# Kernel optimization log

Hardware: AMD Instinct MI355X
Metric: run time of the kernel (lower is better)

The kernel has to match this reference:

```python
import jax, jax.numpy as jnp
import numpy as np

B, T, I, H, O = 64, 1024, 512, 768, 512


def setup_inputs() -> dict:
    key = jax.random.key(0)
    ks = jax.random.split(key, 8)
    x_seq = jax.random.normal(ks[0], (B, T, I), dtype=jnp.float32)
    s = 0.02
    # Gate order along the 4H axis: f, i, g, o (matches the torch module's gates).
    Wx_f = jax.random.normal(ks[1], (4 * H, I), dtype=jnp.float32) * s
    Wh_f = jax.random.normal(ks[2], (4 * H, H), dtype=jnp.float32) * s
    Wx_b = jax.random.normal(ks[3], (4 * H, I), dtype=jnp.float32) * s
    Wh_b = jax.random.normal(ks[4], (4 * H, H), dtype=jnp.float32) * s
    # forget-gate bias init to 1.0 (f_Wxf.bias / b_Wxf.bias), rest 0
    b_gate = jnp.concatenate([jnp.ones((H,), jnp.float32), jnp.zeros((3 * H,), jnp.float32)])
    b_f = b_gate
    b_b = b_gate
    Why = jax.random.normal(ks[5], (O, 2 * H), dtype=jnp.float32) * s
    by = jnp.zeros((O,), jnp.float32)
    return {"x_seq": x_seq, "Wx_f": Wx_f, "Wh_f": Wh_f, "b_f": b_f,
            "Wx_b": Wx_b, "Wh_b": Wh_b, "b_b": b_b, "Why": Why, "by": by}


def _lstm_dir(x, Wx, Wh, b):
    # Precompute all input-to-gate projections in one fused GEMM over time.
    xp = jnp.einsum('bti,gi->btg', x, Wx) + b  # (B, T, 4H)

    def step(carry, xp_t):
        h, c = carry
        z = xp_t + h @ Wh.T                     # (B, 4H)
        f = jax.nn.sigmoid(z[:, 0 * H:1 * H])
        i = jax.nn.sigmoid(z[:, 1 * H:2 * H])
        g = jnp.tanh(z[:, 2 * H:3 * H])
        o = jax.nn.sigmoid(z[:, 3 * H:4 * H])
        c = f * c + i * g
        h = o * jnp.tanh(c)
        return (h, c), None

    h0 = jnp.zeros((x.shape[0], H), x.dtype)
    c0 = jnp.zeros((x.shape[0], H), x.dtype)
    (h, c), _ = jax.lax.scan(step, (h0, c0), jnp.swapaxes(xp, 0, 1))
    return h, c


def reference(x_seq, Wx_f, Wh_f, b_f, Wx_b, Wh_b, b_b, Why, by):
    h_fwd, c_fwd = _lstm_dir(x_seq, Wx_f, Wh_f, b_f)
    h_bwd, c_bwd = _lstm_dir(x_seq[:, ::-1, :], Wx_b, Wh_b, b_b)
    h_combined = jnp.concatenate([h_fwd, h_bwd], axis=1)  # (B, 2H)
    out = h_combined @ Why.T + by
    return out, h_fwd, c_fwd, h_bwd, c_bwd
```

## Files before the change

kernel.cpp:

```cpp
#include <hip/hip_runtime.h>
#include <hip/hip_cooperative_groups.h>

namespace cg = cooperative_groups;

#define B_ 64
#define T_ 1024
#define I_ 512
#define H_ 768
#define O_ 512
#define G4 3072
#define JB 16
#define NJ 48
#define NWGS 192

typedef short short8 __attribute__((ext_vector_type(8)));
typedef float f32x4 __attribute__((ext_vector_type(4)));
typedef int int4v __attribute__((ext_vector_type(4)));

#define XBF_BYTES  (67108864)
#define WCAT_BYTES (15728640)
#define HBUF_BYTES (393216)

__device__ __forceinline__ unsigned short f32_to_bf16(float f) {
    union { float f; unsigned int u; } v; v.f = f;
    unsigned int r = v.u + 0x7fffu + ((v.u >> 16) & 1u);
    return (unsigned short)(r >> 16);
}
__device__ __forceinline__ float sigmoid_f(float x) { return 1.0f / (1.0f + __expf(-x)); }
__device__ __forceinline__ float tanh_f(float x) {
    float e = __expf(2.0f * x);
    return 1.0f - 2.0f / (e + 1.0f);
}

__device__ __forceinline__ void glds16(const void* g, void* l) {
    __builtin_amdgcn_global_load_lds(
        (const __attribute__((address_space(1))) unsigned int*)g,
        (__attribute__((address_space(3))) unsigned int*)l, 16, 0, 0);
}

__device__ __forceinline__ void ldsbar() {
    asm volatile("s_waitcnt lgkmcnt(0)" ::: "memory");
    __builtin_amdgcn_sched_barrier(0);
    __builtin_amdgcn_s_barrier();
    __builtin_amdgcn_sched_barrier(0);
}

__global__ void prep_x_kernel(const float* __restrict__ x, unsigned short* __restrict__ xb) {
    const size_t n = (size_t)B_ * T_ * 64;
    for (size_t i = (size_t)blockIdx.x * blockDim.x + threadIdx.x; i < n;
         i += (size_t)gridDim.x * blockDim.x) {
        int b  = (int)(i >> 16);
        int t  = (int)((i >> 6) & 1023);
        int kb = (int)(i & 63);
        const float4 v0 = *(const float4*)(x + i * 8);
        const float4 v1 = *(const float4*)(x + i * 8 + 4);
        short8 o;
        o[0] = (short)f32_to_bf16(v0.x); o[1] = (short)f32_to_bf16(v0.y);
        o[2] = (short)f32_to_bf16(v0.z); o[3] = (short)f32_to_bf16(v0.w);
        o[4] = (short)f32_to_bf16(v1.x); o[5] = (short)f32_to_bf16(v1.y);
        o[6] = (short)f32_to_bf16(v1.z); o[7] = (short)f32_to_bf16(v1.w);
        *(short8*)(xb + (((size_t)t * 64 + kb) * 64 + b) * 8) = o;
    }
}

__global__ void prep_w_kernel(const float* __restrict__ Wx_f, const float* __restrict__ Wh_f,
                              const float* __restrict__ Wx_b, const float* __restrict__ Wh_b,
                              unsigned short* __restrict__ w2, unsigned short* __restrict__ h2,
                              unsigned* __restrict__ bar) {
    const size_t n = (size_t)2 * G4 * 160;
    for (size_t i = (size_t)blockIdx.x * blockDim.x + threadIdx.x; i < n;
         i += (size_t)gridDim.x * blockDim.x) {
        int dir = (int)(i / 491520);
        int r2  = (int)(i % 491520);
        int row = r2 / 160;
        int kb  = r2 % 160;
        const float* Wx = dir ? Wx_b : Wx_f;
        const float* Wh = dir ? Wh_b : Wh_f;
        const float* src = (kb < 64) ? (Wx + (size_t)row * I_ + kb * 8)
                                     : (Wh + (size_t)row * H_ + (kb - 64) * 8);
        const float4 v0 = *(const float4*)(src);
        const float4 v1 = *(const float4*)(src + 4);
        short8 o;
        o[0] = (short)f32_to_bf16(v0.x); o[1] = (short)f32_to_bf16(v0.y);
        o[2] = (short)f32_to_bf16(v0.z); o[3] = (short)f32_to_bf16(v0.w);
        o[4] = (short)f32_to_bf16(v1.x); o[5] = (short)f32_to_bf16(v1.y);
        o[6] = (short)f32_to_bf16(v1.z); o[7] = (short)f32_to_bf16(v1.w);
        *(short8*)(w2 + (((size_t)dir * 160 + kb) * G4 + row) * 8) = o;
        if (i < 24576) {
            short8 z = {0,0,0,0,0,0,0,0};
            *(short8*)(h2 + i * 8) = z;
        }
        if (i < 512) bar[i] = 0u;
    }
}

__global__ void __launch_bounds__(512, 1)
bilstm_kernel(const float* __restrict__ bias_f, const float* __restrict__ bias_b,
              const unsigned short* __restrict__ xb, const unsigned short* __restrict__ w2,
              unsigned short* h2, unsigned* bar, float* d_out) {
    __shared__ unsigned short x_lds[64 * 32 * 8];
    __shared__ unsigned short h_lds[96 * 32 * 8];
    __shared__ float z_lds[4][32][17];
    __shared__ float c_tile[32][16];

    const int tid   = threadIdx.x;
    const int wg    = blockIdx.x;
    const int dir   = wg / 96;
    const int rem   = wg % 96;
    const int bh    = rem / NJ;
    const int jb    = rem % NJ;
    const int j0    = jb * JB;
    const int wave  = tid >> 6;
    const int lane  = tid & 63;
    const int gate  = wave & 3;
    const int mhalf = wave >> 2;
    const int quad  = lane >> 4;
    const int lrow  = lane & 15;
    const int m0l   = mhalf * 16 + lrow;

    c_tile[tid >> 4][tid & 15] = 0.0f;

    const float bias_r = (dir ? bias_b : bias_f)[gate * H_ + j0 + lrow];
    const int wrow = gate * H_ + j0 + lrow;

    short8 wxr[16];
#pragma unroll
    for (int ks = 0; ks < 16; ++ks)
        wxr[ks] = *(const short8*)(w2 + (((size_t)dir * 160 + ks * 4 + quad) * G4 + wrow) * 8);
    short8 wh[24];
#pragma unroll
    for (int ks = 0; ks < 24; ++ks)
        wh[ks] = *(const short8*)(w2 + (((size_t)dir * 160 + 64 + ks * 4 + quad) * G4 + wrow) * 8);

    const int group = dir * 2 + bh;
    unsigned* mybar = bar + (group * 4 + (jb & 3)) * 32;
    unsigned* barbase = bar + group * 4 * 32;

    const int src_off = (tid >> 5) * 1024 + bh * 512 + (tid & 31) * 16;

    char* const lds_wb   = (char*)x_lds + wave * 1024;
    char* const lds_mine = (char*)h_lds + tid * 16;
    const unsigned short* vax = x_lds + quad * 256 + m0l * 8;
    const unsigned short* vah = h_lds + quad * 256 + m0l * 8;

    {
        const int tx0 = dir ? (T_ - 1) : 0;
        const char* xsrc = (const char*)(xb + (size_t)tx0 * 32768) + src_off;
#pragma unroll
        for (int k = 0; k < 4; ++k) glds16(xsrc + k * 16384, lds_wb + k * 8192);
    }
    __syncthreads();

    for (int t = 0; t < T_; ++t) {
        const int pb = (t + 1) & 1;
        const int cb = t & 1;

        f32x4 acc0; acc0[0] = bias_r; acc0[1] = bias_r; acc0[2] = bias_r; acc0[3] = bias_r;
        f32x4 acc1; acc1[0] = 0.f; acc1[1] = 0.f; acc1[2] = 0.f; acc1[3] = 0.f;

        if (tid == 0 && t) {
            const unsigned tgt = (unsigned)(NJ * t);
            for (;;) {
                unsigned ssum = 0;
#pragma unroll
                for (int i = 0; i < 4; ++i)
                    ssum += __hip_atomic_load(barbase + i * 32, __ATOMIC_RELAXED,
                                              __HIP_MEMORY_SCOPE_AGENT);
                if (ssum >= tgt) break;
                __builtin_amdgcn_s_sleep(1);
            }
        }
#pragma unroll
        for (int ks = 0; ks < 8; ++ks) {
            short8 a0 = *(const short8*)(vax + ks * 1024);
            if (ks & 1) acc1 = __builtin_amdgcn_mfma_f32_16x16x32_bf16(a0, wxr[ks], acc1, 0, 0, 0);
            else        acc0 = __builtin_amdgcn_mfma_f32_16x16x32_bf16(a0, wxr[ks], acc0, 0, 0, 0);
        }
        asm volatile("" ::: "memory");
        __syncthreads();

        const char* hp = (const char*)(h2 + (size_t)(dir * 2 + pb) * 49152) + src_off;
        int4v u0, u1, u2, u3, u4, u5;
        asm volatile("global_load_dwordx4 %0, %1, off sc1" : "=v"(u0) : "v"(hp));
        asm volatile("global_load_dwordx4 %0, %1, off sc1" : "=v"(u1) : "v"(hp + 16384));
        asm volatile("global_load_dwordx4 %0, %1, off sc1" : "=v"(u2) : "v"(hp + 32768));
        asm volatile("global_load_dwordx4 %0, %1, off sc1" : "=v"(u3) : "v"(hp + 49152));
        asm volatile("global_load_dwordx4 %0, %1, off sc1" : "=v"(u4) : "v"(hp + 65536));
        asm volatile("global_load_dwordx4 %0, %1, off sc1" : "=v"(u5) : "v"(hp + 81920));

#pragma unroll
        for (int ks = 8; ks < 16; ++ks) {
            short8 a0 = *(const short8*)(vax + ks * 1024);
            if (ks & 1) acc1 = __builtin_amdgcn_mfma_f32_16x16x32_bf16(a0, wxr[ks], acc1, 0, 0, 0);
            else        acc0 = __builtin_amdgcn_mfma_f32_16x16x32_bf16(a0, wxr[ks], acc0, 0, 0, 0);
        }

        asm volatile("s_waitcnt vmcnt(5)" ::: "memory");
        *(int4v*)(lds_mine) = u0;
        asm volatile("s_waitcnt vmcnt(4)" ::: "memory");
        *(int4v*)(lds_mine + 8192) = u1;
        asm volatile("s_waitcnt vmcnt(3)" ::: "memory");
        *(int4v*)(lds_mine + 16384) = u2;
        asm volatile("s_waitcnt vmcnt(2)" ::: "memory");
        *(int4v*)(lds_mine + 24576) = u3;
        asm volatile("s_waitcnt vmcnt(1)" ::: "memory");
        *(int4v*)(lds_mine + 32768) = u4;
        asm volatile("s_waitcnt vmcnt(0)" ::: "memory");
        *(int4v*)(lds_mine + 40960) = u5;

        ldsbar();

        if (t + 1 < T_) {
            const int tx2 = dir ? (T_ - 2 - t) : (t + 1);
            const char* xsrc = (const char*)(xb + (size_t)tx2 * 32768) + src_off;
#pragma unroll
            for (int k = 0; k < 4; ++k) glds16(xsrc + k * 16384, lds_wb + k * 8192);
        }

#pragma unroll
        for (int ks = 0; ks < 24; ++ks) {
            short8 a0 = *(const short8*)(vah + ks * 1024);
            if (ks & 1) acc1 = __builtin_amdgcn_mfma_f32_16x16x32_bf16(a0, wh[ks], acc1, 0, 0, 0);
            else        acc0 = __builtin_amdgcn_mfma_f32_16x16x32_bf16(a0, wh[ks], acc0, 0, 0, 0);
        }
        f32x4 zv = acc0 + acc1;

#pragma unroll
        for (int r = 0; r < 4; ++r)
            z_lds[gate][mhalf * 16 + quad * 4 + r][lrow] = zv[r];
        ldsbar();

        {
            unsigned short* hw = h2 + (size_t)(dir * 2 + cb) * 49152;
            const int gb  = tid >> 4;
            const int gj  = tid & 15;
            const int gjj = j0 + gj;
            const int bg  = bh * 32 + gb;
            float f0 = sigmoid_f(z_lds[0][gb][gj]);
            float i0 = sigmoid_f(z_lds[1][gb][gj]);
            float g0 = tanh_f(z_lds[2][gb][gj]);
            float o0 = sigmoid_f(z_lds[3][gb][gj]);
            float c0 = f0 * c_tile[gb][gj] + i0 * g0;
            c_tile[gb][gj] = c0;
            float h0 = o0 * tanh_f(c0);
            unsigned hv = (unsigned)f32_to_bf16(h0);
            unsigned ov = __shfl_xor(hv, 1);
            if (!(gj & 1)) {
                unsigned pack = hv | (ov << 16);
                unsigned* dst = (unsigned*)(hw + ((gjj >> 3) * 64 + bg) * 8 + (gjj & 7));
                __hip_atomic_store(dst, pack, __ATOMIC_RELAXED, __HIP_MEMORY_SCOPE_AGENT);
            }
            if (t == T_ - 1) {
                int hoff = 32768 + dir * 98304;
                d_out[hoff + bg * H_ + gjj]         = h0;
                d_out[hoff + 49152 + bg * H_ + gjj] = c0;
            }
        }
        __syncthreads();

        if (tid == 0)
            __hip_atomic_fetch_add(mybar, 1u, __ATOMIC_RELAXED, __HIP_MEMORY_SCOPE_AGENT);
    }
}

__global__ void proj_kernel(float* __restrict__ out, const float* __restrict__ Why,
                            const float* __restrict__ by) {
    __shared__ float hc[2 * H_];
    int b = blockIdx.x;
    const float* hf = out + 32768 + b * H_;
    const float* hb = out + 32768 + 98304 + b * H_;
    for (int i = threadIdx.x; i < H_; i += 256) { hc[i] = hf[i]; hc[H_ + i] = hb[i]; }
    __syncthreads();
    for (int o = threadIdx.x; o < O_; o += 256) {
        const float* wr = Why + (size_t)o * (2 * H_);
        float s = by[o];
        for (int k = 0; k < 2 * H_; k += 4) {
            float4 w = *(const float4*)(wr + k);
            s += w.x * hc[k] + w.y * hc[k + 1] + w.z * hc[k + 2] + w.w * hc[k + 3];
        }
        out[b * O_ + o] = s;
    }
}

extern "C" void kernel_launch(void* const* d_in, const int* in_sizes, int n_in,
                              void* d_out, int out_size, void* d_ws, size_t ws_size,
                              hipStream_t stream) {
    const float* x    = (const float*)d_in[0];
    const float* Wx_f = (const float*)d_in[1];
    const float* Wh_f = (const float*)d_in[2];
    const float* b_f  = (const float*)d_in[3];
    const float* Wx_b = (const float*)d_in[4];
    const float* Wh_b = (const float*)d_in[5];
    const float* b_b  = (const float*)d_in[6];
    const float* Why  = (const float*)d_in[7];
    const float* by   = (const float*)d_in[8];
    float* out = (float*)d_out;

    char* ws = (char*)d_ws;
    unsigned short* xbp = (unsigned short*)(ws);
    unsigned short* w2  = (unsigned short*)(ws + XBF_BYTES);
    unsigned short* h2  = (unsigned short*)(ws + XBF_BYTES + WCAT_BYTES);
    unsigned*       bar = (unsigned*)(ws + XBF_BYTES + WCAT_BYTES + HBUF_BYTES);

    prep_x_kernel<<<8192, 256, 0, stream>>>(x, xbp);
    prep_w_kernel<<<4096, 256, 0, stream>>>(Wx_f, Wh_f, Wx_b, Wh_b, w2, h2, bar);

    void* args[] = {(void*)&b_f, (void*)&b_b, (void*)&xbp, (void*)&w2,
                    (void*)&h2, (void*)&bar, (void*)&out};
    hipLaunchCooperativeKernel((void*)bilstm_kernel, dim3(NWGS), dim3(512), args, 0, stream);

    proj_kernel<<<B_, 256, 0, stream>>>(out, Why, by);
}
```

Baseline: 3.334 ms.

## Split K across wave halves to halve per-wave weight registers

Each group of four waves now covers half the K range (input and hidden) for both 16-row batch halves, instead of the full K range for one batch half. This halves the weight registers each wave holds, and the launch bounds are raised to allow two blocks per CU. The two partial gate sums are written to separate LDS buffers and added before the activations. The staggered vmcnt waits before the LDS stores of h are collapsed into a single wait. The added LDS traffic and the extra partial-sum reduction are small. Since the grid of 192 cooperative blocks was already resident, a second block per CU may bring little benefit.

```diff
diff --git a/kernel.cpp b/kernel.cpp
--- a/kernel.cpp
+++ b/kernel.cpp
@@ -94,13 +94,13 @@
     }
 }
 
-__global__ void __launch_bounds__(512, 1)
+__global__ void __launch_bounds__(512, 2)
 bilstm_kernel(const float* __restrict__ bias_f, const float* __restrict__ bias_b,
               const unsigned short* __restrict__ xb, const unsigned short* __restrict__ w2,
               unsigned short* h2, unsigned* bar, float* d_out) {
     __shared__ unsigned short x_lds[64 * 32 * 8];
     __shared__ unsigned short h_lds[96 * 32 * 8];
-    __shared__ float z_lds[4][32][17];
+    __shared__ float z_part[2][4][32][17];
     __shared__ float c_tile[32][16];
 
     const int tid   = threadIdx.x;
@@ -113,24 +113,23 @@
     const int wave  = tid >> 6;
     const int lane  = tid & 63;
     const int gate  = wave & 3;
-    const int mhalf = wave >> 2;
+    const int khalf = wave >> 2;
     const int quad  = lane >> 4;
     const int lrow  = lane & 15;
-    const int m0l   = mhalf * 16 + lrow;
 
     c_tile[tid >> 4][tid & 15] = 0.0f;
 
-    const float bias_r = (dir ? bias_b : bias_f)[gate * H_ + j0 + lrow];
     const int wrow = gate * H_ + j0 + lrow;
-
-    short8 wxr[16];
-#pragma unroll
-    for (int ks = 0; ks < 16; ++ks)
-        wxr[ks] = *(const short8*)(w2 + (((size_t)dir * 160 + ks * 4 + quad) * G4 + wrow) * 8);
-    short8 wh[24];
-#pragma unroll
-    for (int ks = 0; ks < 24; ++ks)
-        wh[ks] = *(const short8*)(w2 + (((size_t)dir * 160 + 64 + ks * 4 + quad) * G4 + wrow) * 8);
+    const float bias_r = khalf ? 0.0f : (dir ? bias_b : bias_f)[wrow];
+
+    short8 wxr[8];
+#pragma unroll
+    for (int ks = 0; ks < 8; ++ks)
+        wxr[ks] = *(const short8*)(w2 + (((size_t)dir * 160 + khalf * 32 + ks * 4 + quad) * G4 + wrow) * 8);
+    short8 whr[12];
+#pragma unroll
+    for (int ks = 0; ks < 12; ++ks)
+        whr[ks] = *(const short8*)(w2 + (((size_t)dir * 160 + 64 + khalf * 48 + ks * 4 + quad) * G4 + wrow) * 8);
 
     const int group = dir * 2 + bh;
     unsigned* mybar = bar + (group * 4 + (jb & 3)) * 32;
@@ -140,8 +139,8 @@
 
     char* const lds_wb   = (char*)x_lds + wave * 1024;
     char* const lds_mine = (char*)h_lds + tid * 16;
-    const unsigned short* vax = x_lds + quad * 256 + m0l * 8;
-    const unsigned short* vah = h_lds + quad * 256 + m0l * 8;
+    const unsigned short* vax = x_lds + (khalf * 32 + quad) * 256 + lrow * 8;
+    const unsigned short* vah = h_lds + (khalf * 48 + quad) * 256 + lrow * 8;
 
     {
         const int tx0 = dir ? (T_ - 1) : 0;
@@ -155,8 +154,8 @@
         const int pb = (t + 1) & 1;
         const int cb = t & 1;
 
-        f32x4 acc0; acc0[0] = bias_r; acc0[1] = bias_r; acc0[2] = bias_r; acc0[3] = bias_r;
-        f32x4 acc1; acc1[0] = 0.f; acc1[1] = 0.f; acc1[2] = 0.f; acc1[3] = 0.f;
+        f32x4 accA; accA[0] = bias_r; accA[1] = bias_r; accA[2] = bias_r; accA[3] = bias_r;
+        f32x4 accB = accA;
 
         if (tid == 0 && t) {
             const unsigned tgt = (unsigned)(NJ * t);
@@ -171,10 +170,11 @@
             }
         }
 #pragma unroll
-        for (int ks = 0; ks < 8; ++ks) {
+        for (int ks = 0; ks < 4; ++ks) {
             short8 a0 = *(const short8*)(vax + ks * 1024);
-            if (ks & 1) acc1 = __builtin_amdgcn_mfma_f32_16x16x32_bf16(a0, wxr[ks], acc1, 0, 0, 0);
-            else        acc0 = __builtin_amdgcn_mfma_f32_16x16x32_bf16(a0, wxr[ks], acc0, 0, 0, 0);
+            short8 a1 = *(const short8*)(vax + ks * 1024 + 128);
+            accA = __builtin_amdgcn_mfma_f32_16x16x32_bf16(a0, wxr[ks], accA, 0, 0, 0);
+            accB = __builtin_amdgcn_mfma_f32_16x16x32_bf16(a1, wxr[ks], accB, 0, 0, 0);
         }
         asm volatile("" ::: "memory");
         __syncthreads();
@@ -189,24 +189,20 @@
         asm volatile("global_load_dwordx4 %0, %1, off sc1" : "=v"(u5) : "v"(hp + 81920));
 
 #pragma unroll
-        for (int ks = 8; ks < 16; ++ks) {
+        for (int ks = 4; ks < 8; ++ks) {
             short8 a0 = *(const short8*)(vax + ks * 1024);
-            if (ks & 1) acc1 = __builtin_amdgcn_mfma_f32_16x16x32_bf16(a0, wxr[ks], acc1, 0, 0, 0);
-            else        acc0 = __builtin_amdgcn_mfma_f32_16x16x32_bf16(a0, wxr[ks], acc0, 0, 0, 0);
-        }
-
-        asm volatile("s_waitcnt vmcnt(5)" ::: "memory");
-        *(int4v*)(lds_mine) = u0;
-        asm volatile("s_waitcnt vmcnt(4)" ::: "memory");
-        *(int4v*)(lds_mine + 8192) = u1;
-        asm volatile("s_waitcnt vmcnt(3)" ::: "memory");
-        *(int4v*)(lds_mine + 16384) = u2;
-        asm volatile("s_waitcnt vmcnt(2)" ::: "memory");
-        *(int4v*)(lds_mine + 24576) = u3;
-        asm volatile("s_waitcnt vmcnt(1)" ::: "memory");
-        *(int4v*)(lds_mine + 32768) = u4;
+            short8 a1 = *(const short8*)(vax + ks * 1024 + 128);
+            accA = __builtin_amdgcn_mfma_f32_16x16x32_bf16(a0, wxr[ks], accA, 0, 0, 0);
+            accB = __builtin_amdgcn_mfma_f32_16x16x32_bf16(a1, wxr[ks], accB, 0, 0, 0);
+        }
+
         asm volatile("s_waitcnt vmcnt(0)" ::: "memory");
-        *(int4v*)(lds_mine + 40960) = u5;
+        *(int4v*)(lds_mine)          = u0;
+        *(int4v*)(lds_mine +  8192)  = u1;
+        *(int4v*)(lds_mine + 16384)  = u2;
+        *(int4v*)(lds_mine + 24576)  = u3;
+        *(int4v*)(lds_mine + 32768)  = u4;
+        *(int4v*)(lds_mine + 40960)  = u5;
 
         ldsbar();
 
@@ -218,16 +214,18 @@
         }
 
 #pragma unroll
-        for (int ks = 0; ks < 24; ++ks) {
+        for (int ks = 0; ks < 12; ++ks) {
             short8 a0 = *(const short8*)(vah + ks * 1024);
-            if (ks & 1) acc1 = __builtin_amdgcn_mfma_f32_16x16x32_bf16(a0, wh[ks], acc1, 0, 0, 0);
-            else        acc0 = __builtin_amdgcn_mfma_f32_16x16x32_bf16(a0, wh[ks], acc0, 0, 0, 0);
-        }
-        f32x4 zv = acc0 + acc1;
-
-#pragma unroll
-        for (int r = 0; r < 4; ++r)
-            z_lds[gate][mhalf * 16 + quad * 4 + r][lrow] = zv[r];
+            short8 a1 = *(const short8*)(vah + ks * 1024 + 128);
+            accA = __builtin_amdgcn_mfma_f32_16x16x32_bf16(a0, whr[ks], accA, 0, 0, 0);
+            accB = __builtin_amdgcn_mfma_f32_16x16x32_bf16(a1, whr[ks], accB, 0, 0, 0);
+        }
+
+#pragma unroll
+        for (int r = 0; r < 4; ++r) {
+            z_part[khalf][gate][quad * 4 + r][lrow]      = accA[r];
+            z_part[khalf][gate][16 + quad * 4 + r][lrow] = accB[r];
+        }
         ldsbar();
 
         {
@@ -236,10 +234,10 @@
             const int gj  = tid & 15;
             const int gjj = j0 + gj;
             const int bg  = bh * 32 + gb;
-            float f0 = sigmoid_f(z_lds[0][gb][gj]);
-            float i0 = sigmoid_f(z_lds[1][gb][gj]);
-            float g0 = tanh_f(z_lds[2][gb][gj]);
-            float o0 = sigmoid_f(z_lds[3][gb][gj]);
+            float f0 = sigmoid_f(z_part[0][0][gb][gj] + z_part[1][0][gb][gj]);
+            float i0 = sigmoid_f(z_part[0][1][gb][gj] + z_part[1][1][gb][gj]);
+            float g0 = tanh_f(   z_part[0][2][gb][gj] + z_part[1][2][gb][gj]);
+            float o0 = sigmoid_f(z_part[0][3][gb][gj] + z_part[1][3][gb][gj]);
             float c0 = f0 * c_tile[gb][gj] + i0 * g0;
             c_tile[gb][gj] = c0;
             float h0 = o0 * tanh_f(c0);
```

Result: slower. 3.575 ms (+7.2%).
